# Performance work log

Hardware: AMD Instinct MI355X
Metric: run time of the kernel (lower is better)

Reference implementation:

```python
import math
import jax, jax.numpy as jnp
import numpy as np

D_MODEL = 1024
N_HEADS = 16
HEAD_DIM = D_MODEL // N_HEADS  # 64
QDIM = HEAD_DIM // 4           # 16
SPIKE_SLOPE = 5.0
B, S = 2, 2048


def _qweight(r, i, j, k):
    # Hamilton-product weight matrix, identical to QLinear.forward's torch.cat construction.
    return jnp.concatenate([
        jnp.concatenate([r, -i, -j, -k], 1),
        jnp.concatenate([i, r, -k, j], 1),
        jnp.concatenate([j, k, r, -i], 1),
        jnp.concatenate([k, -j, i, r], 1),
    ], 0)


def setup_inputs() -> dict:
    key = jax.random.key(0)
    ks = jax.random.split(key, 20)
    Qo = Qi = D_MODEL // 4  # 256
    p = lambda k, shape, s=0.02: (jax.random.normal(k, shape, dtype=jnp.float32) * s)
    inp = {
        'query': jax.random.normal(ks[0], (B, S, D_MODEL), dtype=jnp.float32),
        'key_in': jax.random.normal(ks[1], (B, S, D_MODEL), dtype=jnp.float32),
        'value': jax.random.normal(ks[2], (B, S, D_MODEL), dtype=jnp.float32),
        'mask': jnp.ones((B, S), dtype=jnp.int32),
        'density_feat': jax.random.normal(ks[3], (B, S, 3), dtype=jnp.float32),
        # q_proj QLinear params
        'wq_r': p(ks[4], (Qo, Qi)), 'wq_i': p(ks[5], (Qo, Qi)),
        'wq_j': p(ks[6], (Qo, Qi)), 'wq_k': p(ks[7], (Qo, Qi)),
        'bq': jnp.zeros((D_MODEL,), jnp.float32),
        # k_proj QLinear params
        'wk_r': p(ks[8], (Qo, Qi)), 'wk_i': p(ks[9], (Qo, Qi)),
        'wk_j': p(ks[10], (Qo, Qi)), 'wk_k': p(ks[11], (Qo, Qi)),
        'bk': jnp.zeros((D_MODEL,), jnp.float32),
        # v_proj / out_proj dense params
        'wv': p(ks[12], (D_MODEL, D_MODEL)), 'bv': jnp.zeros((D_MODEL,), jnp.float32),
        'wo': p(ks[13], (D_MODEL, D_MODEL)), 'bo': jnp.zeros((D_MODEL,), jnp.float32),
        # learned spike threshold (init -1.0 as in torch)
        'threshold': jnp.asarray(-1.0, dtype=jnp.float32),
        # density_mod MLP (use nonzero values so the gate shift is exercised)
        'dm1_w': p(ks[14], (16, 3), 0.5), 'dm1_b': p(ks[15], (16,), 0.1),
        'dm2_w': p(ks[16], (1, 16), 0.5), 'dm2_b': p(ks[17], (1,), 0.1),
    }
    return inp


def reference(query, key_in, value, mask, density_feat,
              wq_r, wq_i, wq_j, wq_k, bq,
              wk_r, wk_i, wk_j, wk_k, bk,
              wv, bv, wo, bo, threshold,
              dm1_w, dm1_b, dm2_w, dm2_b):
    H, hd, Qd = N_HEADS, HEAD_DIM, QDIM
    Bq, Sq, D = query.shape

    Wq = _qweight(wq_r, wq_i, wq_j, wq_k)
    Wk = _qweight(wk_r, wk_i, wk_j, wk_k)
    q = query @ Wq.T + bq
    k = key_in @ Wk.T + bk
    v = value @ wv.T + bv

    # head-major split, matching torch.cat(x.split(hd, -1), dim=0)
    qh = q.reshape(Bq, Sq, H, hd).transpose(2, 0, 1, 3)  # (H,B,S,hd)
    kh = k.reshape(Bq, Sq, H, hd).transpose(2, 0, 1, 3)
    vh = v.reshape(Bq, Sq, H, hd).transpose(2, 0, 1, 3)

    # sum of 4 quaternion-component dot products == full dot product over hd
    scores = jnp.einsum('hbmd,hbnd->hbmn', qh, kh) / math.sqrt(Qd)
    scores = jnp.clip(scores, -6.0, 6.0)

    base_threshold = jax.nn.softplus(threshold)
    h1 = jax.nn.gelu(density_feat @ dm1_w.T + dm1_b, approximate=False)
    d_shift = (h1 @ dm2_w.T + dm2_b)[..., 0]  # (B,N)
    thr = base_threshold + d_shift[None, :, None, :] * 0.1  # (1,B,1,N)

    spike_gate = jax.nn.sigmoid(SPIKE_SLOPE * (scores - thr))
    mod = scores * (1.0 + spike_gate * 2.0)

    m2 = (mask[:, :, None] * mask[:, None, :])[None]  # (1,B,N,N)
    mod = jnp.where(m2 == 0, -10000.0, mod)

    weights = jax.nn.softmax(jnp.clip(mod, -30.0, 30.0), axis=-1)
    # dropout: eval mode (identity)
    out_h = jnp.einsum('hbmn,hbnd->hbmd', weights, vh)
    out = out_h.transpose(1, 2, 0, 3).reshape(Bq, Sq, D)
    return out @ wo.T + bo
```

## Files before the change

kernel.cpp:

```cpp
#include <hip/hip_runtime.h>
#include <stdint.h>
#include <math.h>

#define BB 2
#define SS 2048
#define DM 1024
#define NH 16
#define HD 64
#define MTOT (BB*SS)

typedef __bf16 bf16x8 __attribute__((ext_vector_type(8)));
typedef float  f32x4  __attribute__((ext_vector_type(4)));
typedef uint32_t u32x4 __attribute__((ext_vector_type(4)));

__device__ __forceinline__ unsigned short f2bf(float f) {
  __bf16 h = (__bf16)f;
  return __builtin_bit_cast(unsigned short, h);
}

__device__ __forceinline__ bf16x8 ldsv8(const unsigned short* p) {
  return __builtin_bit_cast(bf16x8, *(const u32x4*)p);
}

__device__ __forceinline__ void gl16(const void* g, void* l) {
  __builtin_amdgcn_global_load_lds(
      (const __attribute__((address_space(1))) uint32_t*)g,
      (__attribute__((address_space(3))) uint32_t*)l, 16, 0, 0);
}

#define MFMA16(a,b,c) __builtin_amdgcn_mfma_f32_16x16x32_bf16((a),(b),(c),0,0,0)

#define C_NEG5L2E  (-7.213475204444817f)
#define C_L2E      (1.4426950408889634f)
#define C_18L2E    (25.968510736001341f)

__global__ __launch_bounds__(256) void cvt_bf16(
    const float* __restrict__ a, const float* __restrict__ b, const float* __restrict__ c,
    unsigned short* __restrict__ ao, unsigned short* __restrict__ bo, unsigned short* __restrict__ co)
{
  const int i8 = (blockIdx.x * 256 + threadIdx.x) * 8;
  {
    const float4 f0 = *(const float4*)(a + i8);
    const float4 f1 = *(const float4*)(a + i8 + 4);
    union { unsigned short us[8]; u32x4 v; } t;
    t.us[0]=f2bf(f0.x); t.us[1]=f2bf(f0.y); t.us[2]=f2bf(f0.z); t.us[3]=f2bf(f0.w);
    t.us[4]=f2bf(f1.x); t.us[5]=f2bf(f1.y); t.us[6]=f2bf(f1.z); t.us[7]=f2bf(f1.w);
    *(u32x4*)(ao + i8) = t.v;
  }
  {
    const float4 f0 = *(const float4*)(b + i8);
    const float4 f1 = *(const float4*)(b + i8 + 4);
    union { unsigned short us[8]; u32x4 v; } t;
    t.us[0]=f2bf(f0.x); t.us[1]=f2bf(f0.y); t.us[2]=f2bf(f0.z); t.us[3]=f2bf(f0.w);
    t.us[4]=f2bf(f1.x); t.us[5]=f2bf(f1.y); t.us[6]=f2bf(f1.z); t.us[7]=f2bf(f1.w);
    *(u32x4*)(bo + i8) = t.v;
  }
  {
    const float4 f0 = *(const float4*)(c + i8);
    const float4 f1 = *(const float4*)(c + i8 + 4);
    union { unsigned short us[8]; u32x4 v; } t;
    t.us[0]=f2bf(f0.x); t.us[1]=f2bf(f0.y); t.us[2]=f2bf(f0.z); t.us[3]=f2bf(f0.w);
    t.us[4]=f2bf(f1.x); t.us[5]=f2bf(f1.y); t.us[6]=f2bf(f1.z); t.us[7]=f2bf(f1.w);
    *(u32x4*)(co + i8) = t.v;
  }
}

__global__ __launch_bounds__(256) void prep_w(
    const float* __restrict__ wqr, const float* __restrict__ wqi,
    const float* __restrict__ wqj, const float* __restrict__ wqk,
    const float* __restrict__ wkr, const float* __restrict__ wki,
    const float* __restrict__ wkj, const float* __restrict__ wkk,
    const float* __restrict__ wv,  const float* __restrict__ wo,
    unsigned short* __restrict__ Wq, unsigned short* __restrict__ Wk,
    unsigned short* __restrict__ Wv, unsigned short* __restrict__ Wo)
{
  const int idx = blockIdx.x * 256 + threadIdx.x;
  const int o = idx >> 10, i = idx & 1023;
  const int br = o >> 8, bc = i >> 8;
  const int ro = o & 255, ci = i & 255;
  const int comp[4][4] = {{0,1,2,3},{1,0,3,2},{2,3,0,1},{3,2,1,0}};
  const float sgn[4][4] = {{1.f,-1.f,-1.f,-1.f},{1.f,1.f,-1.f,1.f},{1.f,1.f,1.f,-1.f},{1.f,-1.f,1.f,1.f}};
  const float* pq[4] = {wqr, wqi, wqj, wqk};
  const float* pk[4] = {wkr, wki, wkj, wkk};
  const int c_ = comp[br][bc];
  const float s_ = sgn[br][bc];
  const int pidx = ro * 256 + ci;
  Wq[idx] = f2bf(s_ * pq[c_][pidx]);
  Wk[idx] = f2bf(s_ * pk[c_][pidx]);
  Wv[idx] = f2bf(wv[idx]);
  Wo[idx] = f2bf(wo[idx]);
}

__global__ __launch_bounds__(256) void prep_thr(
    const float* __restrict__ density, const float* __restrict__ dm1w,
    const float* __restrict__ dm1b, const float* __restrict__ dm2w,
    const float* __restrict__ dm2b, const float* __restrict__ thr_s,
    const int* __restrict__ mask, float2* __restrict__ out)
{
  const int i = blockIdx.x * 256 + threadIdx.x;
  if (i >= BB * SS) return;
  const float x0 = density[i*3+0], x1 = density[i*3+1], x2 = density[i*3+2];
  const float base = log1pf(expf(thr_s[0]));
  float acc = dm2b[0];
  #pragma unroll
  for (int j = 0; j < 16; ++j) {
    const float hj = dm1w[j*3+0]*x0 + dm1w[j*3+1]*x1 + dm1w[j*3+2]*x2 + dm1b[j];
    const float ge = 0.5f * hj * (1.0f + erff(hj * 0.70710678118654752f));
    acc += dm2w[j] * ge;
  }
  const float thr = base + 0.1f * acc;
  out[i] = make_float2(thr * (-C_NEG5L2E),
                       mask[i] ? 1e30f : -30.0f);
}

struct GemmArgs {
  const unsigned short* A[3];
  const unsigned short* W[3];
  const float* bias[3];
  void* out[3];
  float scale[3];
  int omode[3];
};

template<int DB>
__global__ __launch_bounds__(256) void gemm_bt(GemmArgs args)
{
  __shared__ __align__(16) unsigned short lA[DB + 1][128*64];
  __shared__ __align__(16) unsigned short lB[DB + 1][128*64];
  const int z = blockIdx.y;
  const int tid = threadIdx.x;
  const int wid = tid >> 6, lane = tid & 63;
  const int l15 = lane & 15, l4 = lane >> 4;
  const int bm = blockIdx.x & 31, bn = blockIdx.x >> 5;
  const int row0 = bm * 128, col0 = bn * 128;
  const int wm = (wid >> 1) * 64, wn = (wid & 1) * 64;

  const unsigned short* gA[4];
  const unsigned short* gB[4];
  #pragma unroll
  for (int i = 0; i < 4; ++i) {
    const int c = (wid * 4 + i) * 64 + lane;
    const int r = c >> 3, jx = c & 7, j = jx ^ (r & 7);
    gA[i] = args.A[z] + (row0 + r) * 1024 + j * 8;
    gB[i] = args.W[z] + (col0 + r) * 1024 + j * 8;
  }

  f32x4 acc[4][4];
  #pragma unroll
  for (int i = 0; i < 4; ++i)
    #pragma unroll
    for (int j = 0; j < 4; ++j) acc[i][j] = (f32x4){0.f,0.f,0.f,0.f};

  #pragma unroll
  for (int i = 0; i < 4; ++i) {
    gl16(gA[i], &lA[0][(wid * 4 + i) * 512]);
    gl16(gB[i], &lB[0][(wid * 4 + i) * 512]);
  }
  if (DB) __syncthreads();

  for (int kt = 0; kt < 16; ++kt) {
    const int cb = DB ? (kt & 1) : 0;
    if (DB) {
      if (kt < 15) {
        const int nb = cb ^ 1, k0 = (kt + 1) * 64;
        #pragma unroll
        for (int i = 0; i < 4; ++i) {
          gl16(gA[i] + k0, &lA[nb][(wid * 4 + i) * 512]);
          gl16(gB[i] + k0, &lB[nb][(wid * 4 + i) * 512]);
        }
      }
    } else {
      if (kt > 0) {
        const int k0 = kt * 64;
        #pragma unroll
        for (int i = 0; i < 4; ++i) {
          gl16(gA[i] + k0, &lA[0][(wid * 4 + i) * 512]);
          gl16(gB[i] + k0, &lB[0][(wid * 4 + i) * 512]);
        }
      }
      __syncthreads();
    }
    #pragma unroll
    for (int kk = 0; kk < 2; ++kk) {
      const int kl = kk * 32 + l4 * 8;
      bf16x8 af[4], bfb[4];
      #pragma unroll
      for (int mi = 0; mi < 4; ++mi) {
        const int r = wm + mi * 16 + l15;
        af[mi] = ldsv8(&lA[cb][r * 64 + (kl ^ ((r & 7) << 3))]);
      }
      #pragma unroll
      for (int nj = 0; nj < 4; ++nj) {
        const int r = wn + nj * 16 + l15;
        bfb[nj] = ldsv8(&lB[cb][r * 64 + (kl ^ ((r & 7) << 3))]);
      }
      #pragma unroll
      for (int mi = 0; mi < 4; ++mi)
        #pragma unroll
        for (int nj = 0; nj < 4; ++nj)
          acc[mi][nj] = MFMA16(af[mi], bfb[nj], acc[mi][nj]);
    }
    __syncthreads();
  }

  const int om = args.omode[z];
  const float sc = args.scale[z];
  void* Cptr = args.out[z];
  #pragma unroll
  for (int nj = 0; nj < 4; ++nj) {
    const int c = col0 + wn + nj * 16 + l15;
    const float bv_ = args.bias[z][c];
    #pragma unroll
    for (int mi = 0; mi < 4; ++mi) {
      const int rb = row0 + wm + mi * 16 + l4 * 4;
      #pragma unroll
      for (int e = 0; e < 4; ++e) {
        const float val = (acc[mi][nj][e] + bv_) * sc;
        const int r = rb + e;
        if (om == 0) {
          ((unsigned short*)Cptr)[r * 1024 + c] = f2bf(val);
        } else if (om == 2) {
          ((float*)Cptr)[r * 1024 + c] = val;
        } else {
          const int h = c >> 6, d = c & 63, b = r >> 11, s = r & 2047;
          ((unsigned short*)Cptr)[((h * BB + b) * HD + d) * SS + s] = f2bf(val);
        }
      }
    }
  }
}

__global__ __launch_bounds__(256) void attn_kernel(
    const unsigned short* __restrict__ qg, const unsigned short* __restrict__ kg,
    const unsigned short* __restrict__ vT, const float2* __restrict__ klim,
    const int* __restrict__ mask, unsigned short* __restrict__ outg)
{
  __shared__ __align__(16) unsigned short lK[2][64*64];
  __shared__ __align__(16) unsigned short lV[2][64*64];
  __shared__ __align__(16) unsigned short lP[4][16*64];
  const int tid = threadIdx.x;
  const int wid = tid >> 6, lane = tid & 63;
  const int l15 = lane & 15, l4 = lane >> 4;
  const int hb = blockIdx.x & 31, qb = blockIdx.x >> 5;
  const int h = hb >> 1, b = hb & 1;
  const int qr0 = qb * 64 + wid * 16;

  const int c0r = tid >> 3, c0j = (tid & 7) * 8;
  const int c1r = c0r + 32;
  const int dK0 = c0r * 64 + (c0j ^ ((c0r & 7) << 3));
  const int dK1 = c1r * 64 + (c0j ^ ((c1r & 7) << 3));
  const unsigned short* kbase = kg + (b * SS) * DM + h * HD;
  const unsigned short* vbase = vT + ((h * BB + b) * HD) * SS;
  const float2* klimb = klim + b * SS;

  bf16x8 aq[2];
  {
    const unsigned short* qs = qg + (b * SS + qr0 + l15) * DM + h * HD + l4 * 8;
    aq[0] = __builtin_bit_cast(bf16x8, *(const u32x4*)qs);
    aq[1] = __builtin_bit_cast(bf16x8, *(const u32x4*)(qs + 32));
  }
  float limq[4];
  #pragma unroll
  for (int e = 0; e < 4; ++e)
    limq[e] = mask[b * SS + qr0 + l4 * 4 + e] ? 1e30f : -30.0f;

  float lrun[4] = {0.f, 0.f, 0.f, 0.f};
  f32x4 o[4];
  #pragma unroll
  for (int d = 0; d < 4; ++d) o[d] = (f32x4){0.f,0.f,0.f,0.f};

  unsigned short* lPw = lP[wid];

  u32x4 kr0 = *(const u32x4*)(kbase + c0r * DM + c0j);
  u32x4 kr1 = *(const u32x4*)(kbase + c1r * DM + c0j);
  u32x4 vr0 = *(const u32x4*)(vbase + c0r * SS + c0j);
  u32x4 vr1 = *(const u32x4*)(vbase + c1r * SS + c0j);
  *(u32x4*)&lK[0][dK0] = kr0;
  *(u32x4*)&lK[0][dK1] = kr1;
  *(u32x4*)&lV[0][dK0] = vr0;
  *(u32x4*)&lV[0][dK1] = vr1;
  __syncthreads();

  for (int kb = 0; kb < 32; ++kb) {
    const int cur = kb & 1;
    const unsigned short* lKc = lK[cur];
    const unsigned short* lVc = lV[cur];
    const int n0g = kb * 64;

    if (kb < 31) {
      const int n2 = n0g + 64;
      kr0 = *(const u32x4*)(kbase + (n2 + c0r) * DM + c0j);
      kr1 = *(const u32x4*)(kbase + (n2 + c1r) * DM + c0j);
      vr0 = *(const u32x4*)(vbase + c0r * SS + n2 + c0j);
      vr1 = *(const u32x4*)(vbase + c1r * SS + n2 + c0j);
    }

    float2 kl[4];
    #pragma unroll
    for (int cf = 0; cf < 4; ++cf) kl[cf] = klimb[n0g + cf * 16 + l15];

    f32x4 sv[4];
    __builtin_amdgcn_s_setprio(1);
    #pragma unroll
    for (int cf = 0; cf < 4; ++cf) {
      f32x4 a = (f32x4){0.f,0.f,0.f,0.f};
      #pragma unroll
      for (int kk = 0; kk < 2; ++kk) {
        const int n = cf * 16 + l15;
        bf16x8 bk_ = ldsv8(&lKc[n * 64 + ((kk * 32 + l4 * 8) ^ ((n & 7) << 3))]);
        a = MFMA16(aq[kk], bk_, a);
      }
      sv[cf] = a;
    }
    __builtin_amdgcn_s_setprio(0);

    float pvv[4][4];
    #pragma unroll
    for (int cf = 0; cf < 4; ++cf) {
      #pragma unroll
      for (int e = 0; e < 4; ++e) {
        float s = fminf(fmaxf(sv[cf][e], -6.f), 6.f);
        const float t = __builtin_amdgcn_exp2f(fmaf(s, C_NEG5L2E, kl[cf].x));
        const float g = __builtin_amdgcn_rcpf(1.f + t);
        float md = fmaf(s + s, g, s);
        md = fminf(md, fminf(kl[cf].y, limq[e]));
        const float p = __builtin_amdgcn_exp2f(fmaf(md, C_L2E, -C_18L2E));
        pvv[cf][e] = p;
        lrun[e] += p;
      }
    }

    #pragma unroll
    for (int cf = 0; cf < 4; ++cf)
      #pragma unroll
      for (int e = 0; e < 4; ++e) {
        const int rr = l4 * 4 + e, cc = cf * 16 + l15;
        lPw[rr * 64 + (cc ^ ((rr & 7) << 3))] = f2bf(pvv[cf][e]);
      }
    asm volatile("s_waitcnt lgkmcnt(0)" ::: "memory");
    __builtin_amdgcn_sched_barrier(0);

    bf16x8 pa[2];
    #pragma unroll
    for (int kk = 0; kk < 2; ++kk)
      pa[kk] = ldsv8(&lPw[l15 * 64 + ((kk * 32 + l4 * 8) ^ ((l15 & 7) << 3))]);

    __builtin_amdgcn_s_setprio(1);
    #pragma unroll
    for (int df = 0; df < 4; ++df) {
      #pragma unroll
      for (int kk = 0; kk < 2; ++kk) {
        const int d = df * 16 + l15;
        bf16x8 bv_ = ldsv8(&lVc[d * 64 + ((kk * 32 + l4 * 8) ^ ((d & 7) << 3))]);
        o[df] = MFMA16(pa[kk], bv_, o[df]);
      }
    }
    __builtin_amdgcn_s_setprio(0);

    if (kb < 31) {
      const int nxt = cur ^ 1;
      *(u32x4*)&lK[nxt][dK0] = kr0;
      *(u32x4*)&lK[nxt][dK1] = kr1;
      *(u32x4*)&lV[nxt][dK0] = vr0;
      *(u32x4*)&lV[nxt][dK1] = vr1;
    }
    __syncthreads();
  }

  #pragma unroll
  for (int e = 0; e < 4; ++e) {
    float ls = lrun[e];
    ls += __shfl_xor(ls, 1);
    ls += __shfl_xor(ls, 2);
    ls += __shfl_xor(ls, 4);
    ls += __shfl_xor(ls, 8);
    const float rl = __builtin_amdgcn_rcpf(ls);
    const int r = qr0 + l4 * 4 + e;
    #pragma unroll
    for (int df = 0; df < 4; ++df) {
      outg[(b * SS + r) * DM + h * HD + df * 16 + l15] = f2bf(o[df][e] * rl);
    }
  }
}

extern "C" void kernel_launch(void* const* d_in, const int* in_sizes, int n_in,
                              void* d_out, int out_size, void* d_ws, size_t ws_size,
                              hipStream_t stream)
{
  const float* query   = (const float*)d_in[0];
  const float* key_in  = (const float*)d_in[1];
  const float* value   = (const float*)d_in[2];
  const int*   mask    = (const int*)d_in[3];
  const float* density = (const float*)d_in[4];
  const float* wq_r = (const float*)d_in[5];
  const float* wq_i = (const float*)d_in[6];
  const float* wq_j = (const float*)d_in[7];
  const float* wq_k = (const float*)d_in[8];
  const float* bq   = (const float*)d_in[9];
  const float* wk_r = (const float*)d_in[10];
  const float* wk_i = (const float*)d_in[11];
  const float* wk_j = (const float*)d_in[12];
  const float* wk_k = (const float*)d_in[13];
  const float* bk   = (const float*)d_in[14];
  const float* wv   = (const float*)d_in[15];
  const float* bv   = (const float*)d_in[16];
  const float* wo   = (const float*)d_in[17];
  const float* bo   = (const float*)d_in[18];
  const float* thrs = (const float*)d_in[19];
  const float* dm1w = (const float*)d_in[20];
  const float* dm1b = (const float*)d_in[21];
  const float* dm2w = (const float*)d_in[22];
  const float* dm2b = (const float*)d_in[23];

  char* ws = (char*)d_ws;
  unsigned short* Wq  = (unsigned short*)(ws + ((size_t)0 << 20));
  unsigned short* Wk  = (unsigned short*)(ws + ((size_t)2 << 20));
  unsigned short* Wv  = (unsigned short*)(ws + ((size_t)4 << 20));
  unsigned short* Wo  = (unsigned short*)(ws + ((size_t)6 << 20));
  unsigned short* qbf = (unsigned short*)(ws + ((size_t)8 << 20));
  unsigned short* kbf = (unsigned short*)(ws + ((size_t)16 << 20));
  unsigned short* vT  = (unsigned short*)(ws + ((size_t)24 << 20));
  unsigned short* att = (unsigned short*)(ws + ((size_t)32 << 20));
  float2* klim        = (float2*)(ws + ((size_t)40 << 20));

  unsigned short* qcv = (unsigned short*)d_out;
  unsigned short* kcv = (unsigned short*)d_out + (size_t)MTOT * DM;
  unsigned short* vcv = att;

  cvt_bf16<<<2048, 256, 0, stream>>>(query, key_in, value, qcv, kcv, vcv);
  prep_w<<<4096, 256, 0, stream>>>(wq_r, wq_i, wq_j, wq_k,
                                   wk_r, wk_i, wk_j, wk_k,
                                   wv, wo, Wq, Wk, Wv, Wo);
  prep_thr<<<16, 256, 0, stream>>>(density, dm1w, dm1b, dm2w, dm2b, thrs, mask, klim);

  GemmArgs qkv;
  qkv.A[0] = qcv; qkv.W[0] = Wq; qkv.bias[0] = bq; qkv.out[0] = qbf; qkv.scale[0] = 0.25f; qkv.omode[0] = 0;
  qkv.A[1] = kcv; qkv.W[1] = Wk; qkv.bias[1] = bk; qkv.out[1] = kbf; qkv.scale[1] = 1.0f;  qkv.omode[1] = 0;
  qkv.A[2] = vcv; qkv.W[2] = Wv; qkv.bias[2] = bv; qkv.out[2] = vT;  qkv.scale[2] = 1.0f;  qkv.omode[2] = 1;
  gemm_bt<0><<<dim3(256, 3), 256, 0, stream>>>(qkv);

  attn_kernel<<<1024, 256, 0, stream>>>(qbf, kbf, vT, klim, mask, att);

  GemmArgs og;
  og.A[0] = att; og.W[0] = Wo; og.bias[0] = bo; og.out[0] = d_out; og.scale[0] = 1.0f; og.omode[0] = 2;
  og.A[1] = att; og.W[1] = Wo; og.bias[1] = bo; og.out[1] = d_out; og.scale[1] = 1.0f; og.omode[1] = 2;
  og.A[2] = att; og.W[2] = Wo; og.bias[2] = bo; og.out[2] = d_out; og.scale[2] = 1.0f; og.omode[2] = 2;
  gemm_bt<1><<<dim3(256, 1), 256, 0, stream>>>(og);
}
```

Before: 190.3 us.

## Split attention key blocks across paired waves with LDS reduction of partial outputs

The attention kernel moves from 4 to 8 waves per block. Each pair of waves shares a 16-row query tile and splits every 64-key block into two 32-key halves. Partial outputs and row sums are combined through shared memory at the end. The K/V LDS layouts are reorganised, with interleaved key rows and packed P stores, to fit the half-width tiles. The aim is more latency hiding and more parallel work per CU, at the cost of a final cross-wave reduction, extra syncs and fewer registers per thread.

Measured after the change: 188.3 us. About the same (-1.1%).

```diff
diff --git a/kernel.cpp b/kernel.cpp
--- a/kernel.cpp
+++ b/kernel.cpp
@@ -230,25 +230,29 @@
   }
 }
 
-__global__ __launch_bounds__(256) void attn_kernel(
+__global__ __launch_bounds__(512) void attn_kernel(
     const unsigned short* __restrict__ qg, const unsigned short* __restrict__ kg,
     const unsigned short* __restrict__ vT, const float2* __restrict__ klim,
     const int* __restrict__ mask, unsigned short* __restrict__ outg)
 {
-  __shared__ __align__(16) unsigned short lK[2][64*64];
-  __shared__ __align__(16) unsigned short lV[2][64*64];
-  __shared__ __align__(16) unsigned short lP[4][16*64];
+  __shared__ __align__(16) unsigned short smem[20480];
+  unsigned short* lK = smem;
+  unsigned short* lV = smem + 8192;
+  unsigned short* lP = smem + 16384;
+
   const int tid = threadIdx.x;
   const int wid = tid >> 6, lane = tid & 63;
   const int l15 = lane & 15, l4 = lane >> 4;
+  const int rg = wid >> 1, par = wid & 1;
   const int hb = blockIdx.x & 31, qb = blockIdx.x >> 5;
   const int h = hb >> 1, b = hb & 1;
-  const int qr0 = qb * 64 + wid * 16;
-
-  const int c0r = tid >> 3, c0j = (tid & 7) * 8;
-  const int c1r = c0r + 32;
-  const int dK0 = c0r * 64 + (c0j ^ ((c0r & 7) << 3));
-  const int dK1 = c1r * 64 + (c0j ^ ((c1r & 7) << 3));
+  const int qr0 = qb * 64 + rg * 16;
+
+  const int kcr = tid >> 3, kcj = (tid & 7) * 8;
+  const int vcd = tid >> 3, vck = (tid & 7) * 8;
+  const int kdst = (kcr >> 5) * 2048 + (kcr & 31) * 64 + (kcj ^ ((((kcr & 31) >> 1) & 7) << 3));
+  const int vdst = (vck >> 5) * 2048 + vcd * 32 + ((vck & 31) ^ ((vcd & 3) << 3));
+
   const unsigned short* kbase = kg + (b * SS) * DM + h * HD;
   const unsigned short* vbase = vT + ((h * BB + b) * HD) * SS;
   const float2* klimb = klim + b * SS;
@@ -269,61 +273,53 @@
   #pragma unroll
   for (int d = 0; d < 4; ++d) o[d] = (f32x4){0.f,0.f,0.f,0.f};
 
-  unsigned short* lPw = lP[wid];
-
-  u32x4 kr0 = *(const u32x4*)(kbase + c0r * DM + c0j);
-  u32x4 kr1 = *(const u32x4*)(kbase + c1r * DM + c0j);
-  u32x4 vr0 = *(const u32x4*)(vbase + c0r * SS + c0j);
-  u32x4 vr1 = *(const u32x4*)(vbase + c1r * SS + c0j);
-  *(u32x4*)&lK[0][dK0] = kr0;
-  *(u32x4*)&lK[0][dK1] = kr1;
-  *(u32x4*)&lV[0][dK0] = vr0;
-  *(u32x4*)&lV[0][dK1] = vr1;
+  unsigned short* lPw = lP + wid * 512;
+
+  u32x4 kr = *(const u32x4*)(kbase + kcr * DM + kcj);
+  u32x4 vr = *(const u32x4*)(vbase + vcd * SS + vck);
+  *(u32x4*)&lK[kdst] = kr;
+  *(u32x4*)&lV[vdst] = vr;
   __syncthreads();
 
-  for (int kb = 0; kb < 32; ++kb) {
-    const int cur = kb & 1;
-    const unsigned short* lKc = lK[cur];
-    const unsigned short* lVc = lV[cur];
-    const int n0g = kb * 64;
-
-    if (kb < 31) {
-      const int n2 = n0g + 64;
-      kr0 = *(const u32x4*)(kbase + (n2 + c0r) * DM + c0j);
-      kr1 = *(const u32x4*)(kbase + (n2 + c1r) * DM + c0j);
-      vr0 = *(const u32x4*)(vbase + c0r * SS + n2 + c0j);
-      vr1 = *(const u32x4*)(vbase + c1r * SS + n2 + c0j);
-    }
-
-    float2 kl[4];
-    #pragma unroll
-    for (int cf = 0; cf < 4; ++cf) kl[cf] = klimb[n0g + cf * 16 + l15];
-
-    f32x4 sv[4];
+  for (int pr = 0; pr < 32; ++pr) {
+    const int cur = pr & 1;
+    const unsigned short* lKt = lK + cur * 4096 + par * 2048;
+    const unsigned short* lVt = lV + cur * 4096 + par * 2048;
+    const int n0 = pr * 64 + par * 32;
+
+    if (pr < 31) {
+      const int nn = (pr + 1) * 64;
+      kr = *(const u32x4*)(kbase + (nn + kcr) * DM + kcj);
+      vr = *(const u32x4*)(vbase + vcd * SS + nn + vck);
+    }
+
+    const float4 klA = *(const float4*)(klimb + n0 + 2 * l15);
+
+    f32x4 sv[2];
     __builtin_amdgcn_s_setprio(1);
     #pragma unroll
-    for (int cf = 0; cf < 4; ++cf) {
+    for (int cf = 0; cf < 2; ++cf) {
       f32x4 a = (f32x4){0.f,0.f,0.f,0.f};
-      #pragma unroll
-      for (int kk = 0; kk < 2; ++kk) {
-        const int n = cf * 16 + l15;
-        bf16x8 bk_ = ldsv8(&lKc[n * 64 + ((kk * 32 + l4 * 8) ^ ((n & 7) << 3))]);
-        a = MFMA16(aq[kk], bk_, a);
-      }
+      const int r = 2 * l15 + cf;
+      #pragma unroll
+      for (int kk = 0; kk < 2; ++kk)
+        a = MFMA16(aq[kk], ldsv8(&lKt[r * 64 + ((kk * 32 + l4 * 8) ^ ((l15 & 7) << 3))]), a);
       sv[cf] = a;
     }
     __builtin_amdgcn_s_setprio(0);
 
-    float pvv[4][4];
-    #pragma unroll
-    for (int cf = 0; cf < 4; ++cf) {
+    float pvv[2][4];
+    #pragma unroll
+    for (int cf = 0; cf < 2; ++cf) {
+      const float kth = cf ? klA.z : klA.x;
+      const float klm = cf ? klA.w : klA.y;
       #pragma unroll
       for (int e = 0; e < 4; ++e) {
         float s = fminf(fmaxf(sv[cf][e], -6.f), 6.f);
-        const float t = __builtin_amdgcn_exp2f(fmaf(s, C_NEG5L2E, kl[cf].x));
+        const float t = __builtin_amdgcn_exp2f(fmaf(s, C_NEG5L2E, kth));
         const float g = __builtin_amdgcn_rcpf(1.f + t);
         float md = fmaf(s + s, g, s);
-        md = fminf(md, fminf(kl[cf].y, limq[e]));
+        md = fminf(md, fminf(klm, limq[e]));
         const float p = __builtin_amdgcn_exp2f(fmaf(md, C_L2E, -C_18L2E));
         pvv[cf][e] = p;
         lrun[e] += p;
@@ -331,54 +327,66 @@
     }
 
     #pragma unroll
-    for (int cf = 0; cf < 4; ++cf)
-      #pragma unroll
-      for (int e = 0; e < 4; ++e) {
-        const int rr = l4 * 4 + e, cc = cf * 16 + l15;
-        lPw[rr * 64 + (cc ^ ((rr & 7) << 3))] = f2bf(pvv[cf][e]);
-      }
+    for (int e = 0; e < 4; ++e) {
+      const int rr = l4 * 4 + e;
+      union { unsigned short us[2]; unsigned int u; } pk2;
+      pk2.us[0] = f2bf(pvv[0][e]);
+      pk2.us[1] = f2bf(pvv[1][e]);
+      *(unsigned int*)&lPw[rr * 32 + ((2 * l15) ^ ((rr & 3) << 3))] = pk2.u;
+    }
     asm volatile("s_waitcnt lgkmcnt(0)" ::: "memory");
     __builtin_amdgcn_sched_barrier(0);
 
-    bf16x8 pa[2];
-    #pragma unroll
-    for (int kk = 0; kk < 2; ++kk)
-      pa[kk] = ldsv8(&lPw[l15 * 64 + ((kk * 32 + l4 * 8) ^ ((l15 & 7) << 3))]);
+    const bf16x8 pa = ldsv8(&lPw[l15 * 32 + ((l4 * 8) ^ ((l15 & 3) << 3))]);
 
     __builtin_amdgcn_s_setprio(1);
     #pragma unroll
     for (int df = 0; df < 4; ++df) {
-      #pragma unroll
-      for (int kk = 0; kk < 2; ++kk) {
-        const int d = df * 16 + l15;
-        bf16x8 bv_ = ldsv8(&lVc[d * 64 + ((kk * 32 + l4 * 8) ^ ((d & 7) << 3))]);
-        o[df] = MFMA16(pa[kk], bv_, o[df]);
-      }
+      const int d = df * 16 + l15;
+      o[df] = MFMA16(pa, ldsv8(&lVt[d * 32 + ((l4 * 8) ^ ((d & 3) << 3))]), o[df]);
     }
     __builtin_amdgcn_s_setprio(0);
 
-    if (kb < 31) {
+    if (pr < 31) {
       const int nxt = cur ^ 1;
-      *(u32x4*)&lK[nxt][dK0] = kr0;
-      *(u32x4*)&lK[nxt][dK1] = kr1;
-      *(u32x4*)&lV[nxt][dK0] = vr0;
-      *(u32x4*)&lV[nxt][dK1] = vr1;
+      *(u32x4*)&lK[nxt * 4096 + kdst] = kr;
+      *(u32x4*)&lV[nxt * 4096 + vdst] = vr;
     }
     __syncthreads();
   }
 
-  #pragma unroll
-  for (int e = 0; e < 4; ++e) {
-    float ls = lrun[e];
-    ls += __shfl_xor(ls, 1);
-    ls += __shfl_xor(ls, 2);
-    ls += __shfl_xor(ls, 4);
-    ls += __shfl_xor(ls, 8);
-    const float rl = __builtin_amdgcn_rcpf(ls);
-    const int r = qr0 + l4 * 4 + e;
+  __syncthreads();
+  float* xch = (float*)smem;
+  float* slot = xch + rg * 1280;
+  if (par) {
+    #pragma unroll
+    for (int df = 0; df < 4; ++df)
+      *(f32x4*)&slot[(df * 64 + lane) * 4] = o[df];
+    f32x4 lr;
+    lr[0] = lrun[0]; lr[1] = lrun[1]; lr[2] = lrun[2]; lr[3] = lrun[3];
+    *(f32x4*)&slot[1024 + lane * 4] = lr;
+  }
+  __syncthreads();
+  if (!par) {
     #pragma unroll
     for (int df = 0; df < 4; ++df) {
-      outg[(b * SS + r) * DM + h * HD + df * 16 + l15] = f2bf(o[df][e] * rl);
+      const f32x4 t = *(const f32x4*)&slot[(df * 64 + lane) * 4];
+      o[df][0] += t[0]; o[df][1] += t[1]; o[df][2] += t[2]; o[df][3] += t[3];
+    }
+    const f32x4 lr = *(const f32x4*)&slot[1024 + lane * 4];
+    #pragma unroll
+    for (int e = 0; e < 4; ++e) {
+      float ls = lrun[e] + lr[e];
+      ls += __shfl_xor(ls, 1);
+      ls += __shfl_xor(ls, 2);
+      ls += __shfl_xor(ls, 4);
+      ls += __shfl_xor(ls, 8);
+      const float rl = __builtin_amdgcn_rcpf(ls);
+      const int r = qr0 + l4 * 4 + e;
+      #pragma unroll
+      for (int df = 0; df < 4; ++df) {
+        outg[(b * SS + r) * DM + h * HD + df * 16 + l15] = f2bf(o[df][e] * rl);
+      }
     }
   }
 }
@@ -439,7 +447,7 @@
   qkv.A[2] = vcv; qkv.W[2] = Wv; qkv.bias[2] = bv; qkv.out[2] = vT;  qkv.scale[2] = 1.0f;  qkv.omode[2] = 1;
   gemm_bt<0><<<dim3(256, 3), 256, 0, stream>>>(qkv);
 
-  attn_kernel<<<1024, 256, 0, stream>>>(qbf, kbf, vT, klim, mask, att);
+  attn_kernel<<<1024, 512, 0, stream>>>(qbf, kbf, vT, klim, mask, att);
 
   GemmArgs og;
   og.A[0] = att; og.W[0] = Wo; og.bias[0] = bo; og.out[0] = d_out; og.scale[0] = 1.0f; og.omode[0] = 2;
```
